# Performance work log

Measured on AMD Instinct MI355X. Metric: run time of the kernel, lower is better.

## Reference

```python
import jax, jax.numpy as jnp
import numpy as np

HIDDEN = 1152
NUM_HEADS = 16
HEAD_DIM = HIDDEN // NUM_HEADS  # 72
BATCH, SEQ = 8, 1024


def setup_inputs() -> dict:
    key = jax.random.key(0)
    ks = jax.random.split(key, 9)
    s = 0.02
    return {
        "x": jax.random.normal(ks[0], (BATCH, SEQ, HIDDEN), dtype=jnp.float32),
        "wq": jax.random.normal(ks[1], (HIDDEN, HIDDEN), dtype=jnp.float32) * s,
        "bq": jax.random.normal(ks[2], (HIDDEN,), dtype=jnp.float32) * s,
        "wk": jax.random.normal(ks[3], (HIDDEN, HIDDEN), dtype=jnp.float32) * s,
        "bk": jax.random.normal(ks[4], (HIDDEN,), dtype=jnp.float32) * s,
        "wv": jax.random.normal(ks[5], (HIDDEN, HIDDEN), dtype=jnp.float32) * s,
        "bv": jax.random.normal(ks[6], (HIDDEN,), dtype=jnp.float32) * s,
        "wo": jax.random.normal(ks[7], (HIDDEN, HIDDEN), dtype=jnp.float32) * s,
        "bo": jax.random.normal(ks[8], (HIDDEN,), dtype=jnp.float32) * s,
    }


def reference(x, wq, bq, wk, bk, wv, bv, wo, bo):
    B, S, H = x.shape
    nh, hd = NUM_HEADS, HEAD_DIM
    # projections (weights stored [in, out] to match nn.Linear x @ W^T with W^T precomposed)
    q = (x @ wq + bq).reshape(B, S, nh, hd).transpose(0, 2, 1, 3)  # [B,nh,S,hd]
    k = (x @ wk + bk).reshape(B, S, nh, hd).transpose(0, 2, 1, 3)
    v = (x @ wv + bv).reshape(B, S, nh, hd).transpose(0, 2, 1, 3)
    scale = 1.0 / jnp.sqrt(jnp.asarray(hd, dtype=x.dtype))
    scores = jnp.einsum("bhqd,bhkd->bhqk", q, k) * scale  # [B,nh,S,S]
    attn = jax.nn.softmax(scores, axis=-1)
    out = jnp.einsum("bhqk,bhkd->bhqd", attn, v)  # [B,nh,S,hd]
    out = out.transpose(0, 2, 1, 3).reshape(B, S, H)
    return out @ wo + bo
```

## Files before the change

kernel.cpp:

```cpp
#include <hip/hip_runtime.h>
#include <hip/hip_bf16.h>

#define HIDDEN 1152
#define NUM_HEADS 16
#define BATCH 8
#define SEQ 1024
#define MROWS (BATCH * SEQ)
#define KSTRIDE 104
#define QSCALE_L2E (0.11785113019775793f * 1.4426950408889634f)

typedef __attribute__((ext_vector_type(8))) short short8;
typedef __attribute__((ext_vector_type(4))) float f32x4;

__device__ inline short f2bf(float x) {
  unsigned u = __float_as_uint(x);
  unsigned r = (u + 0x7FFFu + ((u >> 16) & 1u)) >> 16;
  return (short)(r & 0xFFFFu);
}

__device__ inline float fexp2(float x) { return __builtin_exp2f(x); }

__device__ inline void gload16(const void* g, void* l) {
  __builtin_amdgcn_global_load_lds(
      (const __attribute__((address_space(1))) void*)g,
      (__attribute__((address_space(3))) void*)l, 16, 0, 0);
}

__global__ __launch_bounds__(256) void k_cvtx(const float* __restrict__ X,
                                              short* __restrict__ Xb) {
  const size_t base = ((size_t)blockIdx.x * 256 + threadIdx.x) * 8;
  float4 a = *(const float4*)(X + base);
  float4 b = *(const float4*)(X + base + 4);
  short8 o = {f2bf(a.x), f2bf(a.y), f2bf(a.z), f2bf(a.w),
              f2bf(b.x), f2bf(b.y), f2bf(b.z), f2bf(b.w)};
  *(short8*)(Xb + base) = o;
}

__global__ __launch_bounds__(256) void k_cvtw(const float* __restrict__ W0,
                                              const float* __restrict__ W1,
                                              const float* __restrict__ W2,
                                              const float* __restrict__ W3,
                                              short* __restrict__ Wt) {
  __shared__ float T[64][65];
  const float* W = (blockIdx.z == 0) ? W0 : (blockIdx.z == 1) ? W1
                 : (blockIdx.z == 2) ? W2 : W3;
  short* dst = Wt + (size_t)blockIdx.z * HIDDEN * HIDDEN;
  const int n0 = blockIdx.x * 64, k0 = blockIdx.y * 64;
  const int tid = threadIdx.x;
  for (int t = tid; t < 4096; t += 256) {
    int r = t >> 6, c = t & 63;
    T[r][c] = W[(size_t)(k0 + r) * HIDDEN + n0 + c];
  }
  __syncthreads();
  for (int t = tid; t < 4096; t += 256) {
    int r = t >> 6, c = t & 63;
    dst[(size_t)(n0 + r) * HIDDEN + k0 + c] = f2bf(T[c][r]);
  }
}

__global__ __launch_bounds__(256) void k_kpad(short* __restrict__ Kp) {
  const int r = blockIdx.x * 256 + threadIdx.x;
  const short8 z = {0, 0, 0, 0, 0, 0, 0, 0};
  short* p = Kp + (size_t)r * KSTRIDE + 72;
  *(short8*)(p) = z;
  *(short8*)(p + 8) = z;
  *(short8*)(p + 16) = z;
}

__global__ __launch_bounds__(256) void k_vzero(short* __restrict__ Vt) {
  const int t = blockIdx.x * 256 + threadIdx.x;
  const int bh = t >> 10;
  const int off = (t & 1023) * 8;
  const short8 z = {0, 0, 0, 0, 0, 0, 0, 0};
  *(short8*)(Vt + (size_t)bh * 81920 + 73728 + off) = z;
}

__global__ __launch_bounds__(512) void k_gemm_qkv(
    const short* __restrict__ A, const short* __restrict__ Bt,
    const float* __restrict__ bq, const float* __restrict__ bk,
    const float* __restrict__ bv, short* __restrict__ Qb,
    short* __restrict__ Kp, short* __restrict__ Vt) {
  __shared__ __align__(16) short SM[24576];
  short* As = SM;
  short* Bs = SM + 16384;
  const int tid = threadIdx.x;
  const int lane = tid & 63;
  const int wid = tid >> 6;
  const int wr = wid >> 1, wc = wid & 1;
  const int flat = blockIdx.y * 27 + blockIdx.x;
  const int rid = (flat & 7) * 108 + (flat >> 3);
  const int row0 = (rid / 27) << 8;
  const int colTile = rid % 27;
  const int col0 = colTile << 7;
  const int l15 = lane & 15, lh = lane >> 4;
  const int lr8 = lane >> 3;
  const int csrc = ((lane & 7) ^ lr8) << 3;

  const f32x4 fz = {0.f, 0.f, 0.f, 0.f};
  f32x4 acc[4][4];
#pragma unroll
  for (int m = 0; m < 4; ++m)
#pragma unroll
    for (int n = 0; n < 4; ++n) acc[m][n] = fz;

  for (int k0 = 0; k0 < HIDDEN; k0 += 64) {
#pragma unroll
    for (int i = 0; i < 4; ++i) {
      const int c = (wid << 2) + i;
      const int r = (c << 3) + lr8;
      gload16(A + (size_t)(row0 + r) * HIDDEN + k0 + csrc, (void*)(As + (c << 9)));
    }
#pragma unroll
    for (int i = 0; i < 2; ++i) {
      const int c = (wid << 1) + i;
      const int r = (c << 3) + lr8;
      gload16(Bt + (size_t)(col0 + r) * HIDDEN + k0 + csrc, (void*)(Bs + (c << 9)));
    }
    __syncthreads();
#pragma unroll
    for (int ks = 0; ks < 2; ++ks) {
      short8 af[4], bfr[4];
#pragma unroll
      for (int m = 0; m < 4; ++m) {
        const int r = (wr << 6) + (m << 4) + l15;
        const int off = ((ks << 6) + (lh << 4)) ^ ((r & 7) << 4);
        af[m] = *(const short8*)((const char*)As + r * 128 + off);
      }
#pragma unroll
      for (int n = 0; n < 4; ++n) {
        const int r = (wc << 6) + (n << 4) + l15;
        const int off = ((ks << 6) + (lh << 4)) ^ ((r & 7) << 4);
        bfr[n] = *(const short8*)((const char*)Bs + r * 128 + off);
      }
      __builtin_amdgcn_s_setprio(1);
#pragma unroll
      for (int m = 0; m < 4; ++m)
#pragma unroll
        for (int n = 0; n < 4; ++n)
          acc[m][n] = __builtin_amdgcn_mfma_f32_16x16x32_bf16(af[m], bfr[n], acc[m][n], 0, 0, 0);
      __builtin_amdgcn_s_setprio(0);
    }
    __syncthreads();
  }

  const int cseg = colTile / 9;
  const int cwithin = (colTile % 9) << 7;
  if (cseg < 2) {
    short* dst = (cseg == 0) ? Qb : Kp;
    const float* bias = (cseg == 0) ? bq : bk;
    const float scl = (cseg == 0) ? QSCALE_L2E : 1.0f;
    const int rstride = (cseg == 0) ? 72 : KSTRIDE;
#pragma unroll
    for (int n = 0; n < 4; ++n) {
      const int c = cwithin + (wc << 6) + (n << 4) + l15;
      const int h = c / 72;
      const int d = c - h * 72;
      const float bvx = bias[c];
#pragma unroll
      for (int m = 0; m < 4; ++m)
#pragma unroll
        for (int i = 0; i < 4; ++i) {
          const int r = row0 + (wr << 6) + (m << 4) + (lh << 2) + i;
          const int b = r >> 10, s = r & 1023;
          dst[(size_t)((((b << 4) + h) << 10) + s) * rstride + d] =
              f2bf((acc[m][n][i] + bvx) * scl);
        }
    }
  } else {
    const int b = row0 >> 10;
    const int sb = row0 & 1023;
    short* Td = SM;
#pragma unroll
    for (int p = 0; p < 2; ++p) {
      if (wc == p) {
#pragma unroll
        for (int n = 0; n < 4; ++n) {
          const int ci = n * 16 + l15;
          const float bvx = bv[cwithin + p * 64 + ci];
#pragma unroll
          for (int m = 0; m < 4; ++m) {
            const int r0 = (wr << 6) + (m << 4) + (lh << 2);
            short4 o;
            o.x = f2bf(acc[m][n][0] + bvx);
            o.y = f2bf(acc[m][n][1] + bvx);
            o.z = f2bf(acc[m][n][2] + bvx);
            o.w = f2bf(acc[m][n][3] + bvx);
            *(short4*)(Td + ci * 264 + r0) = o;
          }
        }
      }
      __syncthreads();
      {
        const int ci = tid >> 3;
        const int part = tid & 7;
        const int cg = cwithin + p * 64 + ci;
        const int h = cg / 72;
        const int d = cg - h * 72;
        short* dstp = Vt + (((size_t)(((b << 4) + h) * 80 + d)) << 10) + sb + part * 32;
        const short* srcp = Td + ci * 264 + part * 32;
#pragma unroll
        for (int k = 0; k < 4; ++k)
          *(short8*)(dstp + k * 8) = *(const short8*)(srcp + k * 8);
      }
      __syncthreads();
    }
  }
}

__global__ __launch_bounds__(256) void k_gemm_o(const short* __restrict__ A,
                                                const short* __restrict__ Bt,
                                                const float* __restrict__ bias,
                                                float* __restrict__ C) {
  __shared__ __align__(16) short As[8192];
  __shared__ __align__(16) short Bs[8192];
  const int tid = threadIdx.x;
  const int lane = tid & 63;
  const int wid = tid >> 6;
  const int wr = wid >> 1, wc = wid & 1;
  const int flat = blockIdx.y * 9 + blockIdx.x;
  const int rid = (flat & 7) * 72 + (flat >> 3);
  const int row0 = (rid / 9) << 7;
  const int col0 = (rid % 9) << 7;
  const int l15 = lane & 15, lh = lane >> 4;
  const int lr8 = lane >> 3;
  const int csrc = ((lane & 7) ^ lr8) << 3;

  const f32x4 fz = {0.f, 0.f, 0.f, 0.f};
  f32x4 acc[4][4];
#pragma unroll
  for (int m = 0; m < 4; ++m)
#pragma unroll
    for (int n = 0; n < 4; ++n) acc[m][n] = fz;

  for (int k0 = 0; k0 < HIDDEN; k0 += 64) {
#pragma unroll
    for (int i = 0; i < 4; ++i) {
      const int chunk = (wid << 2) + i;
      const int r = (chunk << 3) + lr8;
      gload16(A + (size_t)(row0 + r) * HIDDEN + k0 + csrc, (void*)(As + (chunk << 9)));
      gload16(Bt + (size_t)(col0 + r) * HIDDEN + k0 + csrc, (void*)(Bs + (chunk << 9)));
    }
    __syncthreads();
#pragma unroll
    for (int ks = 0; ks < 2; ++ks) {
      short8 af[4], bfr[4];
#pragma unroll
      for (int m = 0; m < 4; ++m) {
        const int r = (wr << 6) + (m << 4) + l15;
        const int off = ((ks << 6) + (lh << 4)) ^ ((r & 7) << 4);
        af[m] = *(const short8*)((const char*)As + r * 128 + off);
      }
#pragma unroll
      for (int n = 0; n < 4; ++n) {
        const int r = (wc << 6) + (n << 4) + l15;
        const int off = ((ks << 6) + (lh << 4)) ^ ((r & 7) << 4);
        bfr[n] = *(const short8*)((const char*)Bs + r * 128 + off);
      }
      __builtin_amdgcn_s_setprio(1);
#pragma unroll
      for (int m = 0; m < 4; ++m)
#pragma unroll
        for (int n = 0; n < 4; ++n)
          acc[m][n] = __builtin_amdgcn_mfma_f32_16x16x32_bf16(af[m], bfr[n], acc[m][n], 0, 0, 0);
      __builtin_amdgcn_s_setprio(0);
    }
    __syncthreads();
  }

#pragma unroll
  for (int n = 0; n < 4; ++n) {
    const int c = col0 + (wc << 6) + (n << 4) + l15;
    const float bvx = bias[c];
#pragma unroll
    for (int m = 0; m < 4; ++m)
#pragma unroll
      for (int i = 0; i < 4; ++i) {
        const int r = row0 + (wr << 6) + (m << 4) + (lh << 2) + i;
        C[(size_t)r * HIDDEN + c] = acc[m][n][i] + bvx;
      }
  }
}

__global__ __launch_bounds__(256, 4) void k_attn(const short* __restrict__ Qg,
                                                 const short* __restrict__ Kp,
                                                 const short* __restrict__ Vt,
                                                 short* __restrict__ Og) {
  __shared__ __align__(16) short Ks[64 * KSTRIDE];
  __shared__ __align__(16) short Vs[80 * 64];
  __shared__ __align__(16) short Ps[4 * 16 * 72];
  const int tid = threadIdx.x, lane = tid & 63, wid = tid >> 6;
  const int l15 = lane & 15, lh = lane >> 4;
  const int id = blockIdx.x;
  const int rid = (id & 7) * 128 + (id >> 3);
  const int bh = rid >> 3;
  const int q0 = (rid & 7) << 7;
  const short8 sz = {0, 0, 0, 0, 0, 0, 0, 0};
  const f32x4 fz = {0.f, 0.f, 0.f, 0.f};

  short8 qf[2][3];
#pragma unroll
  for (int m = 0; m < 2; ++m)
#pragma unroll
    for (int ks = 0; ks < 3; ++ks) {
      const int row = q0 + wid * 32 + m * 16 + l15;
      const int e0 = ks * 32 + lh * 8;
      if (e0 < 72)
        qf[m][ks] = *(const short8*)(Qg + ((size_t)bh * 1024 + row) * 72 + e0);
      else
        qf[m][ks] = sz;
    }

  float mrun[2] = {-1e30f, -1e30f};
  float lrun[2] = {0.f, 0.f};
  f32x4 oacc[2][5];
#pragma unroll
  for (int m = 0; m < 2; ++m)
#pragma unroll
    for (int no = 0; no < 5; ++no) oacc[m][no] = fz;

  const char* kgb = (const char*)Kp + ((size_t)bh * 1024) * (KSTRIDE * 2);
  const char* vgb = (const char*)Vt + (size_t)bh * 163840;

  for (int kt = 0; kt < 16; ++kt) {
    const char* kg = kgb + (size_t)kt * 64 * (KSTRIDE * 2);
    for (int c = wid; c < 13; c += 4)
      gload16(kg + c * 1024 + lane * 16, (char*)Ks + c * 1024);
    for (int c = wid; c < 10; c += 4) {
      const int p = c * 1024 + lane * 16;
      const int d = p >> 7;
      const int sc16 = (lane & 7) ^ (d & 7);
      gload16(vgb + (size_t)d * 2048 + kt * 128 + sc16 * 16, (char*)Vs + c * 1024);
    }
    __syncthreads();

#pragma unroll
    for (int m = 0; m < 2; ++m) {
      f32x4 sa[4];
#pragma unroll
      for (int n = 0; n < 4; ++n) sa[n] = fz;
#pragma unroll
      for (int ks = 0; ks < 3; ++ks) {
        short8 kf[4];
#pragma unroll
        for (int n = 0; n < 4; ++n)
          kf[n] = *(const short8*)((const char*)Ks + (n * 16 + l15) * 208 + ks * 64 + lh * 16);
        __builtin_amdgcn_s_setprio(1);
#pragma unroll
        for (int n = 0; n < 4; ++n)
          sa[n] = __builtin_amdgcn_mfma_f32_16x16x32_bf16(kf[n], qf[m][ks], sa[n], 0, 0, 0);
        __builtin_amdgcn_s_setprio(0);
      }

      float mx = sa[0][0];
#pragma unroll
      for (int n = 0; n < 4; ++n)
#pragma unroll
        for (int i = 0; i < 4; ++i) mx = fmaxf(mx, sa[n][i]);
      mx = fmaxf(mx, __shfl_xor(mx, 16));
      mx = fmaxf(mx, __shfl_xor(mx, 32));

      const bool skip = __all(mx <= mrun[m] + 8.0f);
      if (!skip) {
        const float nm = fmaxf(mrun[m], mx);
        const float corr = fexp2(mrun[m] - nm);
        lrun[m] *= corr;
        mrun[m] = nm;
        float c0 = __shfl(corr, lh * 4 + 0);
        float c1 = __shfl(corr, lh * 4 + 1);
        float c2 = __shfl(corr, lh * 4 + 2);
        float c3 = __shfl(corr, lh * 4 + 3);
        const f32x4 cv = {c0, c1, c2, c3};
#pragma unroll
        for (int no = 0; no < 5; ++no) oacc[m][no] *= cv;
      }

      float ps = 0.f;
#pragma unroll
      for (int n = 0; n < 4; ++n)
#pragma unroll
        for (int i = 0; i < 4; ++i) {
          const float p = fexp2(sa[n][i] - mrun[m]);
          sa[n][i] = p;
          ps += p;
        }
      ps += __shfl_xor(ps, 16);
      ps += __shfl_xor(ps, 32);
      lrun[m] += ps;

#pragma unroll
      for (int n = 0; n < 4; ++n) {
        unsigned w0 = __builtin_amdgcn_perm(__float_as_uint(sa[n][1]),
                                            __float_as_uint(sa[n][0]), 0x07060302u);
        unsigned w1 = __builtin_amdgcn_perm(__float_as_uint(sa[n][3]),
                                            __float_as_uint(sa[n][2]), 0x07060302u);
        uint2 w = {w0, w1};
        *(uint2*)((char*)Ps + wid * 2304 + l15 * 144 + n * 32 + lh * 8) = w;
      }

#pragma unroll
      for (int ks = 0; ks < 2; ++ks) {
        const short8 pa = *(const short8*)((const char*)Ps + wid * 2304 + l15 * 144 + ks * 64 + lh * 16);
        short8 vb[5];
        const int cc = ((ks << 2) + lh) ^ (l15 & 7);
#pragma unroll
        for (int no = 0; no < 5; ++no)
          vb[no] = *(const short8*)((const char*)Vs + no * 2048 + l15 * 128 + cc * 16);
        __builtin_amdgcn_s_setprio(1);
#pragma unroll
        for (int no = 0; no < 5; ++no)
          oacc[m][no] = __builtin_amdgcn_mfma_f32_16x16x32_bf16(pa, vb[no], oacc[m][no], 0, 0, 0);
        __builtin_amdgcn_s_setprio(0);
      }
    }
    __syncthreads();
  }

  const int b = bh >> 4, h = bh & 15;
#pragma unroll
  for (int m = 0; m < 2; ++m) {
    const float il = 1.0f / lrun[m];
    float inv[4];
#pragma unroll
    for (int i = 0; i < 4; ++i) inv[i] = __shfl(il, lh * 4 + i);
#pragma unroll
    for (int no = 0; no < 5; ++no) {
      const int d = no * 16 + l15;
      if (d < 72) {
#pragma unroll
        for (int i = 0; i < 4; ++i) {
          const int s = q0 + wid * 32 + m * 16 + lh * 4 + i;
          Og[((size_t)(b * 1024 + s)) * HIDDEN + h * 72 + d] = f2bf(oacc[m][no][i] * inv[i]);
        }
      }
    }
  }
}

extern "C" void kernel_launch(void* const* d_in, const int* in_sizes, int n_in,
                              void* d_out, int out_size, void* d_ws, size_t ws_size,
                              hipStream_t stream) {
  const float* x  = (const float*)d_in[0];
  const float* wq = (const float*)d_in[1];
  const float* bq = (const float*)d_in[2];
  const float* wk = (const float*)d_in[3];
  const float* bk = (const float*)d_in[4];
  const float* wv = (const float*)d_in[5];
  const float* bv = (const float*)d_in[6];
  const float* wo = (const float*)d_in[7];
  const float* bo = (const float*)d_in[8];

  char* ws = (char*)d_ws;
  short* xb = (short*)ws;
  short* wT = (short*)(ws + 18874368);
  short* Qb = (short*)(ws + 29491200);
  short* Kp = (short*)(ws + 48365568);
  short* Vt = (short*)(ws + 75628544);
  const size_t WSZ = (size_t)HIDDEN * HIDDEN;

  k_cvtx<<<4608, 256, 0, stream>>>(x, xb);
  k_cvtw<<<dim3(18, 18, 4), 256, 0, stream>>>(wq, wk, wv, wo, wT);
  k_kpad<<<512, 256, 0, stream>>>(Kp);
  k_vzero<<<512, 256, 0, stream>>>(Vt);

  k_gemm_qkv<<<dim3(27, 32), 512, 0, stream>>>(xb, wT, bq, bk, bv, Qb, Kp, Vt);
  k_attn<<<1024, 256, 0, stream>>>(Qb, Kp, Vt, xb);
  k_gemm_o<<<dim3(9, 64), 256, 0, stream>>>(xb, wT + 3 * WSZ, bo, (float*)d_out);
}
```

Measured before the change: 228.0 us.

## Compute softmax row sums via ones column in V MFMA; fuse prep kernels

```diff
diff --git a/kernel.cpp b/kernel.cpp
--- a/kernel.cpp
+++ b/kernel.cpp
@@ -26,14 +26,33 @@
       (__attribute__((address_space(3))) void*)l, 16, 0, 0);
 }
 
-__global__ __launch_bounds__(256) void k_cvtx(const float* __restrict__ X,
-                                              short* __restrict__ Xb) {
-  const size_t base = ((size_t)blockIdx.x * 256 + threadIdx.x) * 8;
-  float4 a = *(const float4*)(X + base);
-  float4 b = *(const float4*)(X + base + 4);
-  short8 o = {f2bf(a.x), f2bf(a.y), f2bf(a.z), f2bf(a.w),
-              f2bf(b.x), f2bf(b.y), f2bf(b.z), f2bf(b.w)};
-  *(short8*)(Xb + base) = o;
+__global__ __launch_bounds__(256) void k_prep(const float* __restrict__ X,
+                                              short* __restrict__ Xb,
+                                              short* __restrict__ Kp,
+                                              short* __restrict__ Vt) {
+  const int bid = blockIdx.x;
+  if (bid < 4608) {
+    const size_t base = ((size_t)bid * 256 + threadIdx.x) * 8;
+    float4 a = *(const float4*)(X + base);
+    float4 b = *(const float4*)(X + base + 4);
+    short8 o = {f2bf(a.x), f2bf(a.y), f2bf(a.z), f2bf(a.w),
+                f2bf(b.x), f2bf(b.y), f2bf(b.z), f2bf(b.w)};
+    *(short8*)(Xb + base) = o;
+  } else if (bid < 5120) {
+    const int r = (bid - 4608) * 256 + threadIdx.x;
+    const short8 z = {0, 0, 0, 0, 0, 0, 0, 0};
+    short* p = Kp + (size_t)r * KSTRIDE + 72;
+    *(short8*)(p) = z;
+    *(short8*)(p + 8) = z;
+    *(short8*)(p + 16) = z;
+  } else {
+    const int t = (bid - 5120) * 256 + threadIdx.x;
+    const int bh = t >> 10;
+    const int off = (t & 1023) * 8;
+    const short o = ((t & 1023) >> 7) == 0 ? (short)0x3F80 : (short)0;
+    short8 v = {o, o, o, o, o, o, o, o};
+    *(short8*)(Vt + (size_t)bh * 81920 + 73728 + off) = v;
+  }
 }
 
 __global__ __launch_bounds__(256) void k_cvtw(const float* __restrict__ W0,
@@ -56,23 +75,6 @@
     int r = t >> 6, c = t & 63;
     dst[(size_t)(n0 + r) * HIDDEN + k0 + c] = f2bf(T[c][r]);
   }
-}
-
-__global__ __launch_bounds__(256) void k_kpad(short* __restrict__ Kp) {
-  const int r = blockIdx.x * 256 + threadIdx.x;
-  const short8 z = {0, 0, 0, 0, 0, 0, 0, 0};
-  short* p = Kp + (size_t)r * KSTRIDE + 72;
-  *(short8*)(p) = z;
-  *(short8*)(p + 8) = z;
-  *(short8*)(p + 16) = z;
-}
-
-__global__ __launch_bounds__(256) void k_vzero(short* __restrict__ Vt) {
-  const int t = blockIdx.x * 256 + threadIdx.x;
-  const int bh = t >> 10;
-  const int off = (t & 1023) * 8;
-  const short8 z = {0, 0, 0, 0, 0, 0, 0, 0};
-  *(short8*)(Vt + (size_t)bh * 81920 + 73728 + off) = z;
 }
 
 __global__ __launch_bounds__(512) void k_gemm_qkv(
@@ -311,7 +313,6 @@
     }
 
   float mrun[2] = {-1e30f, -1e30f};
-  float lrun[2] = {0.f, 0.f};
   f32x4 oacc[2][5];
 #pragma unroll
   for (int m = 0; m < 2; ++m)
@@ -351,19 +352,20 @@
         __builtin_amdgcn_s_setprio(0);
       }
 
-      float mx = sa[0][0];
-#pragma unroll
-      for (int n = 0; n < 4; ++n)
-#pragma unroll
-        for (int i = 0; i < 4; ++i) mx = fmaxf(mx, sa[n][i]);
-      mx = fmaxf(mx, __shfl_xor(mx, 16));
-      mx = fmaxf(mx, __shfl_xor(mx, 32));
-
-      const bool skip = __all(mx <= mrun[m] + 8.0f);
-      if (!skip) {
+#define M3(a, b, c) fmaxf(fmaxf((a), (b)), (c))
+      float t0 = M3(sa[0][0], sa[0][1], sa[0][2]);
+      float t1 = M3(sa[0][3], sa[1][0], sa[1][1]);
+      float t2 = M3(sa[1][2], sa[1][3], sa[2][0]);
+      float t3 = M3(sa[2][1], sa[2][2], sa[2][3]);
+      float t4 = M3(sa[3][0], sa[3][1], sa[3][2]);
+      float mx = fmaxf(M3(t0, t1, sa[3][3]), M3(t2, t3, t4));
+#undef M3
+
+      if (__any(mx > mrun[m] + 8.0f)) {
+        mx = fmaxf(mx, __shfl_xor(mx, 16));
+        mx = fmaxf(mx, __shfl_xor(mx, 32));
         const float nm = fmaxf(mrun[m], mx);
         const float corr = fexp2(mrun[m] - nm);
-        lrun[m] *= corr;
         mrun[m] = nm;
         float c0 = __shfl(corr, lh * 4 + 0);
         float c1 = __shfl(corr, lh * 4 + 1);
@@ -374,18 +376,10 @@
         for (int no = 0; no < 5; ++no) oacc[m][no] *= cv;
       }
 
-      float ps = 0.f;
 #pragma unroll
       for (int n = 0; n < 4; ++n)
 #pragma unroll
-        for (int i = 0; i < 4; ++i) {
-          const float p = fexp2(sa[n][i] - mrun[m]);
-          sa[n][i] = p;
-          ps += p;
-        }
-      ps += __shfl_xor(ps, 16);
-      ps += __shfl_xor(ps, 32);
-      lrun[m] += ps;
+        for (int i = 0; i < 4; ++i) sa[n][i] = fexp2(sa[n][i] - mrun[m]);
 
 #pragma unroll
       for (int n = 0; n < 4; ++n) {
@@ -418,10 +412,10 @@
   const int b = bh >> 4, h = bh & 15;
 #pragma unroll
   for (int m = 0; m < 2; ++m) {
-    const float il = 1.0f / lrun[m];
     float inv[4];
 #pragma unroll
-    for (int i = 0; i < 4; ++i) inv[i] = __shfl(il, lh * 4 + i);
+    for (int i = 0; i < 4; ++i)
+      inv[i] = 1.0f / __shfl(oacc[m][4][i], (lane & 48) + 8);
 #pragma unroll
     for (int no = 0; no < 5; ++no) {
       const int d = no * 16 + l15;
@@ -457,10 +451,8 @@
   short* Vt = (short*)(ws + 75628544);
   const size_t WSZ = (size_t)HIDDEN * HIDDEN;
 
-  k_cvtx<<<4608, 256, 0, stream>>>(x, xb);
+  k_prep<<<5632, 256, 0, stream>>>(x, xb, Kp, Vt);
   k_cvtw<<<dim3(18, 18, 4), 256, 0, stream>>>(wq, wk, wv, wo, wT);
-  k_kpad<<<512, 256, 0, stream>>>(Kp);
-  k_vzero<<<512, 256, 0, stream>>>(Vt);
 
   k_gemm_qkv<<<dim3(27, 32), 512, 0, stream>>>(xb, wT, bq, bk, bv, Qb, Kp, Vt);
   k_attn<<<1024, 256, 0, stream>>>(Qb, Kp, Vt, xb);
```

Result: faster. 217.2 us (-4.7%).
